# Optimization experiments

Measured on AMD Instinct MI355X. Metric: run time of the kernel, lower is better.

## Reference

```python
import jax, jax.numpy as jnp
import numpy as np

F, N, C, H, M = 256, 400, 128, 8, 128  # frames, batch*joints, mdl_channels, heads, max_pos
E = C // H


def _layer_norm(z, g, b, eps=1e-5):
    mu = jnp.mean(z, axis=-1, keepdims=True)
    var = jnp.mean((z - mu) ** 2, axis=-1, keepdims=True)
    return (z - mu) * jax.lax.rsqrt(var + eps) * g + b


def setup_inputs() -> dict:
    key = jax.random.key(0)
    ks = jax.random.split(key, 16)
    s = 0.02
    return {
        "x": jax.random.normal(ks[0], (F, N, C), jnp.float32),
        "tree_encoding": jax.random.normal(ks[1], (N, C), jnp.float32),
        "W_qkv": jax.random.normal(ks[2], (3 * C, C), jnp.float32) * s,      # Linear weight (out,in), no bias
        "W_tree_k": jax.random.normal(ks[3], (C, C), jnp.float32) * s,
        "W_tree_v": jax.random.normal(ks[4], (C, C), jnp.float32) * s,
        "emb": jax.random.normal(ks[5], (2 * M + 1, E), jnp.float32) * s,    # distance embedding table
        "W_beta": jax.random.normal(ks[6], (1, 3 * C), jnp.float32) * s,     # lin_beta (out,in), no bias
        "ln1_g": jnp.ones((C,), jnp.float32),
        "ln1_b": jnp.zeros((C,), jnp.float32),
        "ln2_g": jnp.ones((C,), jnp.float32),
        "ln2_b": jnp.zeros((C,), jnp.float32),
        "W1": jax.random.normal(ks[7], (C, C), jnp.float32) * s,
        "b1": jnp.zeros((C,), jnp.float32),
        "W2": jax.random.normal(ks[8], (C, C), jnp.float32) * s,
        "b2": jnp.zeros((C,), jnp.float32),
    }


def reference(x, tree_encoding, W_qkv, W_tree_k, W_tree_v, emb, W_beta,
              ln1_g, ln1_b, ln2_g, ln2_b, W1, b1, W2, b2):
    f, n, c = x.shape
    # qkv projection, no bias
    qkv = x @ W_qkv.T                          # (f, n, 3c)
    q, k, v = jnp.split(qkv, 3, axis=-1)       # each (f, n, c)
    # tree positional encoding added to key/value
    k = k + (tree_encoding @ W_tree_k)[None]
    v = v + (tree_encoding @ W_tree_v)[None]
    # (f, n, c) -> (n, f, h, e): n is the attention batch, f is sequence length
    to_heads = lambda t: t.transpose(1, 0, 2).reshape(n, f, H, E)
    qh, kh, vh = to_heads(q), to_heads(k), to_heads(v)
    # content scores
    qk = jnp.einsum('nlhe,nshe->nhls', qh, kh)
    # relative position bias
    ids = jnp.arange(f)
    dist = jnp.clip(ids[:, None] - ids[None, :], -M, M) + M   # (f, f)
    pe = emb[dist]                                            # (f, f, e)
    qk = qk + jnp.einsum('nlhe,lse->nhls', qh, pe)
    qk = qk + jnp.einsum('nshe,lse->nhls', kh, pe)
    scale = 1.0 / (E ** 0.5)
    att = jax.nn.softmax(qk * scale, axis=-1)                 # (n, h, f, f)
    out = jnp.einsum('nhls,nshe->nlhe', att, vh)              # (n, f, h, e)
    y = out.reshape(n, f, c).transpose(1, 0, 2)               # (f, n, c)
    # gated AddNorm (beta=True): x is residual, y is attention output
    gate = jax.nn.sigmoid(jnp.concatenate([y, x, y - x], axis=-1) @ W_beta.T)
    h1 = _layer_norm(gate * x + (1.0 - gate) * y, ln1_g, ln1_b)
    # FFN (GELU exact, as torch nn.GELU default)
    ff = jax.nn.gelu(h1 @ W1.T + b1, approximate=False) @ W2.T + b2
    return _layer_norm(ff + h1, ln2_g, ln2_b)
```

## Files before the change

### kernel.cpp

```cpp
#include <hip/hip_runtime.h>
#include <math.h>

#define F_DIM 256
#define N_DIM 400
#define C_DIM 128
#define H_DIM 8
#define E_DIM 16
#define ROWS  (F_DIM * N_DIM)
#define SBUF  (N_DIM * H_DIM * F_DIM * E_DIM)

#define S_SCALE 0.6005612043932249f

typedef _Float16 half2_t __attribute__((ext_vector_type(2)));
typedef _Float16 f16x8   __attribute__((ext_vector_type(8)));
typedef float    f32x16  __attribute__((ext_vector_type(16)));
typedef float    f32x4   __attribute__((ext_vector_type(4)));

struct H2x4 { half2_t h[4]; };

__device__ inline f16x8 pack8(float4 a, float4 b) {
    H2x4 t;
    t.h[0] = __builtin_bit_cast(half2_t, __builtin_amdgcn_cvt_pkrtz(a.x, a.y));
    t.h[1] = __builtin_bit_cast(half2_t, __builtin_amdgcn_cvt_pkrtz(a.z, a.w));
    t.h[2] = __builtin_bit_cast(half2_t, __builtin_amdgcn_cvt_pkrtz(b.x, b.y));
    t.h[3] = __builtin_bit_cast(half2_t, __builtin_amdgcn_cvt_pkrtz(b.z, b.w));
    return __builtin_bit_cast(f16x8, t);
}

__device__ inline _Float16 h_rtz(float v) {
    half2_t p = __builtin_bit_cast(half2_t, __builtin_amdgcn_cvt_pkrtz(v, v));
    return p[0];
}

__device__ inline int iclamp256(int v) { return v < 0 ? 0 : (v > 256 ? 256 : v); }

__global__ __launch_bounds__(256) void prep_pack(
    const float* __restrict__ x, const float* __restrict__ Wq,
    const float* __restrict__ emb, const float* __restrict__ te,
    const float* __restrict__ Wtk, const float* __restrict__ Wtv,
    const float* __restrict__ W1, const float* __restrict__ W2,
    _Float16* __restrict__ xh, _Float16* __restrict__ Wqh,
    _Float16* __restrict__ embh, float* __restrict__ tk, float* __restrict__ tv,
    _Float16* __restrict__ W1h, _Float16* __restrict__ W2h)
{
    int bid = blockIdx.x;
    int t   = threadIdx.x;
    if (bid < 6400) {
        int i = (bid * 256 + t) * 8;
        const float4* s = (const float4*)(x + i);
        *(uint4*)(xh + i) = __builtin_bit_cast(uint4, pack8(s[0], s[1]));
    } else if (bid < 6424) {
        int i = ((bid - 6400) * 256 + t) * 8;
        const float4* s = (const float4*)(Wq + i);
        *(uint4*)(Wqh + i) = __builtin_bit_cast(uint4, pack8(s[0], s[1]));
    } else if (bid < 6426) {
        int r = (bid - 6424) * 256 + t;
        if (r > 256) return;
        const float4* er = (const float4*)(emb + r * 16);
        float4 e0 = er[0], e1 = er[1], e2 = er[2], e3 = er[3];
        e0.x *= S_SCALE; e0.y *= S_SCALE; e0.z *= S_SCALE; e0.w *= S_SCALE;
        e1.x *= S_SCALE; e1.y *= S_SCALE; e1.z *= S_SCALE; e1.w *= S_SCALE;
        e2.x *= S_SCALE; e2.y *= S_SCALE; e2.z *= S_SCALE; e2.w *= S_SCALE;
        e3.x *= S_SCALE; e3.y *= S_SCALE; e3.z *= S_SCALE; e3.w *= S_SCALE;
        *(uint4*)(embh + r * 16)     = __builtin_bit_cast(uint4, pack8(e0, e1));
        *(uint4*)(embh + r * 16 + 8) = __builtin_bit_cast(uint4, pack8(e2, e3));
    } else if (bid < 6826) {
        int n = bid - 6426;
        const float* W = (t < 128) ? Wtk : Wtv;
        float* outp    = (t < 128) ? tk : tv;
        int j = t & 127;
        float acc = 0.f;
        #pragma unroll 4
        for (int c = 0; c < 128; ++c)
            acc += te[n * 128 + c] * W[c * 128 + j];
        outp[n * 128 + j] = acc;
    } else if (bid < 6834) {
        int i = ((bid - 6826) * 256 + t) * 8;
        const float4* s = (const float4*)(W1 + i);
        *(uint4*)(W1h + i) = __builtin_bit_cast(uint4, pack8(s[0], s[1]));
    } else {
        int i = ((bid - 6834) * 256 + t) * 8;
        const float4* s = (const float4*)(W2 + i);
        *(uint4*)(W2h + i) = __builtin_bit_cast(uint4, pack8(s[0], s[1]));
    }
}

__global__ __launch_bounds__(256) void qkv_gemm(
    const _Float16* __restrict__ xh, const _Float16* __restrict__ Wqh,
    const float* __restrict__ tk, const float* __restrict__ tv,
    _Float16* __restrict__ qn, _Float16* __restrict__ kn, _Float16* __restrict__ vn)
{
    int tid  = threadIdx.x;
    int wave = tid >> 6, lane = tid & 63;
    int m32  = lane & 31, khalf = lane >> 5;

    int bid = blockIdx.x;
    int xcd = bid & 7;
    int tt  = bid >> 3;
    int cb  = tt % 6;
    int rp  = (tt / 6) * 8 + xcd;
    int row0 = rp * 64 + (wave & 1) * 32;
    int col0 = cb * 64 + (wave >> 1) * 32;

    const _Float16* xp = xh  + (row0 + m32) * 128 + khalf * 8;
    const _Float16* wp = Wqh + (col0 + m32) * 128 + khalf * 8;

    f32x16 acc;
    #pragma unroll
    for (int i = 0; i < 16; ++i) acc[i] = 0.f;

    #pragma unroll
    for (int k0 = 0; k0 < 128; k0 += 16) {
        f16x8 xa = __builtin_bit_cast(f16x8, *(const uint4*)(xp + k0));
        f16x8 wa = __builtin_bit_cast(f16x8, *(const uint4*)(wp + k0));
        acc = __builtin_amdgcn_mfma_f32_32x32x16_f16(xa, wa, acc, 0, 0, 0);
    }

    int o   = col0 + m32;
    int sec = o >> 7;
    int rem = o & 127;
    #pragma unroll
    for (int reg = 0; reg < 16; ++reg) {
        int r = row0 + (reg & 3) + 8 * (reg >> 2) + 4 * khalf;
        float val = acc[reg];
        if (sec == 0) {
            qn[r * 128 + rem] = h_rtz(val * S_SCALE);
        } else {
            int f = r / 400;
            int n = r - f * 400;
            if (sec == 1) {
                kn[r * 128 + rem] = h_rtz((val + tk[n * 128 + rem]) * S_SCALE);
            } else {
                vn[r * 128 + rem] = (_Float16)(val + tv[n * 128 + rem]);
            }
        }
    }
}

__global__ __launch_bounds__(256) void v_pack(
    const _Float16* __restrict__ vn, _Float16* __restrict__ vT)
{
    __shared__ _Float16 sm[16 * 264];
    int bn = blockIdx.x;
    int n  = bn >> 3, h = bn & 7;
    int t  = threadIdx.x;

    const uint4* src = (const uint4*)(vn + (t * 400 + n) * 128 + h * 16);
    uint4 a = src[0], b = src[1];
    union { uint4 u; _Float16 hv[8]; } ua, ub;
    ua.u = a; ub.u = b;
    #pragma unroll
    for (int e = 0; e < 8; ++e) sm[e * 264 + t]       = ua.hv[e];
    #pragma unroll
    for (int e = 0; e < 8; ++e) sm[(e + 8) * 264 + t] = ub.hv[e];
    __syncthreads();

    #pragma unroll
    for (int k = 0; k < 2; ++k) {
        int idx = (k * 256 + t) * 8;
        int e = idx >> 8, f0 = idx & 255;
        uint4 o = *(const uint4*)(sm + e * 264 + f0);
        *(uint4*)(vT + bn * 4096 + idx) = o;
    }
}

#define R2_STRIDE 258
#define PS_STRIDE 40

__global__ __launch_bounds__(512, 4) void attn_kernel(
    const _Float16* __restrict__ qb, const _Float16* __restrict__ kb,
    const _Float16* __restrict__ vb, const _Float16* __restrict__ embh,
    _Float16* __restrict__ y)
{
    __shared__ __align__(16) _Float16 R2sh[32 * R2_STRIDE];
    __shared__ __align__(16) _Float16 Psh[8 * 32 * PS_STRIDE];

    int tid  = threadIdx.x;
    int wave = tid >> 6, lane = tid & 63;
    int bid  = blockIdx.x;
    int bn   = (bid & 7) * 400 + (bid >> 3);
    int n    = bn >> 3, h = bn & 7;
    int base = bn * 4096;

    int nn  = lane & 31;
    int kh  = lane >> 5;
    int khb = (lane & 32) << 2;
    int cbase = 31 + 4 * kh - nn;
    int dbase = 4 * kh - nn;
    int q16 = (lane >> 4) & 3;

    int nat_off = n * 128 + h * 16 + kh * 8;

    f16x8 aq = __builtin_bit_cast(f16x8,
        *(const uint4*)(qb + (32 * wave + nn) * 51200 + nat_off));

    f16x8 bones;
    #pragma unroll
    for (int i = 0; i < 8; ++i) bones[i] = (_Float16)1.0f;

    f32x4 O[2];
    f32x4 Od[2];
    #pragma unroll
    for (int a = 0; a < 2; ++a)
        #pragma unroll
        for (int r = 0; r < 4; ++r) { O[a][r] = 0.f; Od[a][r] = 0.f; }

    _Float16* psw = Psh + wave * 32 * PS_STRIDE;

    for (int st = 0; st < 8; ++st) {
        f16x8 bk = __builtin_bit_cast(f16x8,
            *(const uint4*)(kb + (32 * st + nn) * 51200 + nat_off));

        auto r2tile = [&](int ct) {
            int erow = 32 * ct + nn; if (erow > 256) erow = 256;
            f16x8 be = __builtin_bit_cast(f16x8,
                *(const uint4*)(embh + erow * 16 + kh * 8));
            f32x16 c2;
            #pragma unroll
            for (int i = 0; i < 16; ++i) c2[i] = 0.f;
            c2 = __builtin_amdgcn_mfma_f32_32x32x16_f16(bk, be, c2, 0, 0, 0);
            int col = 32 * ct + nn;
            if (col <= 256) {
                #pragma unroll
                for (int r = 0; r < 16; ++r) {
                    int srow = (r & 3) + 8 * (r >> 2) + 4 * kh;
                    R2sh[srow * R2_STRIDE + col] = (_Float16)c2[r];
                }
            }
        };
        r2tile(wave);
        if (wave == (st & 7)) r2tile(8);
        __syncthreads();

        f16x8 bv = __builtin_bit_cast(f16x8,
            *(const uint4*)(vb + base + (lane & 15) * 256 + 32 * st + q16 * 8));

        int U0 = 32 * wave - 32 * st + 128;

        int br0 = iclamp256(U0 - 31 + nn);
        int br1 = iclamp256(U0 + 1 + nn);
        f16x8 be0 = __builtin_bit_cast(f16x8,
            *(const uint4*)(embh + br0 * 16 + kh * 8));
        f16x8 be1 = __builtin_bit_cast(f16x8,
            *(const uint4*)(embh + br1 * 16 + kh * 8));
        f32x16 W0, W1;
        #pragma unroll
        for (int i = 0; i < 16; ++i) { W0[i] = 0.f; W1[i] = 0.f; }
        W0 = __builtin_amdgcn_mfma_f32_32x32x16_f16(aq, be0, W0, 0, 0, 0);
        W1 = __builtin_amdgcn_mfma_f32_32x32x16_f16(aq, be1, W1, 0, 0, 0);

        half2_t b1p[8];
        #pragma unroll
        for (int r = 0; r < 16; ++r) {
            int rmr = (r & 3) + 8 * (r >> 2);
            int c   = rmr + cbase;
            int addr = ((c & 31) << 2) + khb;
            int w01 = __builtin_bit_cast(int,
                __builtin_amdgcn_cvt_pkrtz(W0[r], W1[r]));
            half2_t hh = __builtin_bit_cast(half2_t,
                __builtin_amdgcn_ds_bpermute(addr, w01));
            b1p[r >> 1][r & 1] = (c < 32) ? hh[0] : hh[1];
        }

        f32x16 S;
        #pragma unroll
        for (int i = 0; i < 16; ++i) S[i] = 0.f;
        S = __builtin_amdgcn_mfma_f32_32x32x16_f16(aq, bk, S, 0, 0, 0);

        #pragma unroll
        for (int r = 0; r < 16; ++r) {
            int rmr = (r & 3) + 8 * (r >> 2);
            float b1 = (float)b1p[r >> 1][r & 1];
            int d = iclamp256(U0 + rmr + dbase);
            float b2 = (float)R2sh[nn * R2_STRIDE + d];
            float p = __builtin_amdgcn_exp2f(S[r] + b1 + b2);
            int mloc = rmr + 4 * kh;
            psw[mloc * PS_STRIDE + nn] = (_Float16)p;
        }

        #pragma unroll
        for (int a = 0; a < 2; ++a) {
            f16x8 ap = __builtin_bit_cast(f16x8,
                *(const uint4*)(psw + (16 * a + (lane & 15)) * PS_STRIDE + q16 * 8));
            O[a]  = __builtin_amdgcn_mfma_f32_16x16x32_f16(ap, bv,    O[a],  0, 0, 0);
            Od[a] = __builtin_amdgcn_mfma_f32_16x16x32_f16(ap, bones, Od[a], 0, 0, 0);
        }
        __syncthreads();
    }

    #pragma unroll
    for (int a = 0; a < 2; ++a) {
        #pragma unroll
        for (int r = 0; r < 4; ++r) {
            int row  = q16 * 4 + r;
            int lloc = 16 * a + row;
            int lg = 32 * wave + lloc;
            y[(lg * 400 + n) * 128 + h * 16 + (lane & 15)] =
                (_Float16)(O[a][r] / Od[a][r]);
        }
    }
}

__global__ __launch_bounds__(256) void ffn_fused(
    const float* __restrict__ x, const _Float16* __restrict__ yh,
    const float* __restrict__ Wb,
    const float* __restrict__ ln1g, const float* __restrict__ ln1b,
    const _Float16* __restrict__ W1h, const float* __restrict__ b1,
    const _Float16* __restrict__ W2h, const float* __restrict__ b2,
    const float* __restrict__ ln2g, const float* __restrict__ ln2b,
    float* __restrict__ outp)
{
    __shared__ __align__(16) _Float16 h1sh[32 * 136];
    __shared__ __align__(16) _Float16 gsh[32 * 136];
    __shared__ float Cs[32 * 132];

    int tid  = threadIdx.x;
    int rloc = tid >> 3;
    int seg  = (tid & 7) * 16;
    int r    = blockIdx.x * 32 + rloc;

    float xv[16], yv[16];
    {
        const float4* xp = (const float4*)(x + r * 128 + seg);
        float4 x0 = xp[0], x1 = xp[1], x2 = xp[2], x3 = xp[3];
        xv[0]=x0.x; xv[1]=x0.y; xv[2]=x0.z; xv[3]=x0.w;
        xv[4]=x1.x; xv[5]=x1.y; xv[6]=x1.z; xv[7]=x1.w;
        xv[8]=x2.x; xv[9]=x2.y; xv[10]=x2.z; xv[11]=x2.w;
        xv[12]=x3.x; xv[13]=x3.y; xv[14]=x3.z; xv[15]=x3.w;
        const uint4* yp = (const uint4*)(yh + r * 128 + seg);
        uint4 y0 = yp[0], y1 = yp[1];
        union { uint4 u; _Float16 hv[8]; } uy0, uy1;
        uy0.u = y0; uy1.u = y1;
        #pragma unroll
        for (int j = 0; j < 8; ++j) { yv[j] = (float)uy0.hv[j]; yv[8+j] = (float)uy1.hv[j]; }
    }
    float sv = 0.f;
    {
        const float4* w0p = (const float4*)(Wb + seg);
        const float4* w1p = (const float4*)(Wb + 128 + seg);
        const float4* w2p = (const float4*)(Wb + 256 + seg);
        #pragma unroll
        for (int j4 = 0; j4 < 4; ++j4) {
            float4 w0 = w0p[j4], w1 = w1p[j4], w2 = w2p[j4];
            float* w0f = (float*)&w0; float* w1f = (float*)&w1; float* w2f = (float*)&w2;
            #pragma unroll
            for (int jj = 0; jj < 4; ++jj) {
                int j = j4 * 4 + jj;
                sv += yv[j] * w0f[jj] + xv[j] * w1f[jj] + (yv[j] - xv[j]) * w2f[jj];
            }
        }
    }
    #pragma unroll
    for (int off = 4; off > 0; off >>= 1) sv += __shfl_xor(sv, off);
    float gate = 1.0f / (1.0f + __expf(-sv));

    float z[16], s1 = 0.f, s2 = 0.f;
    #pragma unroll
    for (int j = 0; j < 16; ++j) {
        z[j] = gate * xv[j] + (1.0f - gate) * yv[j];
        s1 += z[j]; s2 += z[j] * z[j];
    }
    #pragma unroll
    for (int off = 4; off > 0; off >>= 1) {
        s1 += __shfl_xor(s1, off);
        s2 += __shfl_xor(s2, off);
    }
    float mu  = s1 * (1.0f / 128.0f);
    float var = s2 * (1.0f / 128.0f) - mu * mu;
    float rs  = rsqrtf(var + 1e-5f);

    float h1r[16];
    {
        const float4* gp = (const float4*)(ln1g + seg);
        const float4* bp = (const float4*)(ln1b + seg);
        #pragma unroll
        for (int j4 = 0; j4 < 4; ++j4) {
            float4 gv = gp[j4], bv = bp[j4];
            float* gf = (float*)&gv; float* bf = (float*)&bv;
            #pragma unroll
            for (int jj = 0; jj < 4; ++jj) {
                int j = j4 * 4 + jj;
                h1r[j] = (z[j] - mu) * rs * gf[jj] + bf[jj];
            }
        }
        #pragma unroll
        for (int j = 0; j < 8; ++j) {
            *(uint*)(h1sh + rloc * 136 + seg + 2 * j) = __builtin_bit_cast(uint,
                __builtin_amdgcn_cvt_pkrtz(h1r[2 * j], h1r[2 * j + 1]));
        }
    }
    __syncthreads();

    int wave = tid >> 6, lane = tid & 63;
    int m32  = lane & 31, khalf = lane >> 5;
    int col0 = wave * 32;
    {
        f32x16 acc;
        #pragma unroll
        for (int i = 0; i < 16; ++i) acc[i] = 0.f;
        const _Float16* ap = h1sh + m32 * 136 + khalf * 8;
        const _Float16* wp = W1h + (col0 + m32) * 128 + khalf * 8;
        #pragma unroll
        for (int k0 = 0; k0 < 128; k0 += 16) {
            f16x8 aa = __builtin_bit_cast(f16x8, *(const uint4*)(ap + k0));
            f16x8 wa = __builtin_bit_cast(f16x8, *(const uint4*)(wp + k0));
            acc = __builtin_amdgcn_mfma_f32_32x32x16_f16(aa, wa, acc, 0, 0, 0);
        }
        int   c  = col0 + m32;
        float bi = b1[c];
        #pragma unroll
        for (int reg = 0; reg < 16; ++reg) {
            int row2 = (reg & 3) + 8 * (reg >> 2) + 4 * khalf;
            float v = acc[reg] + bi;
            v = 0.5f * v * (1.0f + erff(v * 0.70710678118654752f));
            gsh[row2 * 136 + c] = (_Float16)v;
        }
    }
    __syncthreads();

    {
        f32x16 acc;
        #pragma unroll
        for (int i = 0; i < 16; ++i) acc[i] = 0.f;
        const _Float16* ap = gsh + m32 * 136 + khalf * 8;
        const _Float16* wp = W2h + (col0 + m32) * 128 + khalf * 8;
        #pragma unroll
        for (int k0 = 0; k0 < 128; k0 += 16) {
            f16x8 aa = __builtin_bit_cast(f16x8, *(const uint4*)(ap + k0));
            f16x8 wa = __builtin_bit_cast(f16x8, *(const uint4*)(wp + k0));
            acc = __builtin_amdgcn_mfma_f32_32x32x16_f16(aa, wa, acc, 0, 0, 0);
        }
        #pragma unroll
        for (int reg = 0; reg < 16; ++reg) {
            int row2 = (reg & 3) + 8 * (reg >> 2) + 4 * khalf;
            Cs[row2 * 132 + col0 + m32] = acc[reg];
        }
    }
    __syncthreads();

    float z2[16];
    float t1 = 0.f, t2 = 0.f;
    #pragma unroll
    for (int j4 = 0; j4 < 4; ++j4) {
        float4 cv = *(const float4*)(Cs + rloc * 132 + seg + j4 * 4);
        float4 bv = *(const float4*)(b2 + seg + j4 * 4);
        float* cf = (float*)&cv; float* bf = (float*)&bv;
        #pragma unroll
        for (int jj = 0; jj < 4; ++jj) {
            int j = j4 * 4 + jj;
            z2[j] = cf[jj] + bf[jj] + h1r[j];
            t1 += z2[j]; t2 += z2[j] * z2[j];
        }
    }
    #pragma unroll
    for (int off = 4; off > 0; off >>= 1) {
        t1 += __shfl_xor(t1, off);
        t2 += __shfl_xor(t2, off);
    }
    float mu2  = t1 * (1.0f / 128.0f);
    float var2 = t2 * (1.0f / 128.0f) - mu2 * mu2;
    float rs2  = rsqrtf(var2 + 1e-5f);
    #pragma unroll
    for (int j4 = 0; j4 < 4; ++j4) {
        float4 gv = *(const float4*)(ln2g + seg + j4 * 4);
        float4 bv = *(const float4*)(ln2b + seg + j4 * 4);
        float* gf = (float*)&gv; float* bf = (float*)&bv;
        float4 ov;
        float* of = (float*)&ov;
        #pragma unroll
        for (int jj = 0; jj < 4; ++jj) {
            int j = j4 * 4 + jj;
            of[jj] = (z2[j] - mu2) * rs2 * gf[jj] + bf[jj];
        }
        *(float4*)(outp + r * 128 + seg + j4 * 4) = ov;
    }
}

extern "C" void kernel_launch(void* const* d_in, const int* in_sizes, int n_in,
                              void* d_out, int out_size, void* d_ws, size_t ws_size,
                              hipStream_t stream)
{
    const float* x     = (const float*)d_in[0];
    const float* te    = (const float*)d_in[1];
    const float* Wqkv  = (const float*)d_in[2];
    const float* Wtk   = (const float*)d_in[3];
    const float* Wtv   = (const float*)d_in[4];
    const float* emb   = (const float*)d_in[5];
    const float* Wbeta = (const float*)d_in[6];
    const float* ln1g  = (const float*)d_in[7];
    const float* ln1b  = (const float*)d_in[8];
    const float* ln2g  = (const float*)d_in[9];
    const float* ln2b  = (const float*)d_in[10];
    const float* W1    = (const float*)d_in[11];
    const float* b1    = (const float*)d_in[12];
    const float* W2    = (const float*)d_in[13];
    const float* b2    = (const float*)d_in[14];
    float* outp = (float*)d_out;

    float* ws = (float*)d_ws;
    float* tk = ws;
    float* tv = ws + 51200;
    float* qb_region = ws + 102400;
    float* kb_region = qb_region + SBUF;
    float* vb_region = kb_region + SBUF;
    float* yb        = vb_region + SBUF;

    _Float16* qnat = (_Float16*)qb_region;
    _Float16* knat = (_Float16*)kb_region;
    _Float16* vnat = (_Float16*)vb_region;
    _Float16* vT   = (_Float16*)(vb_region + SBUF / 2);
    _Float16* embh = (_Float16*)(qb_region + SBUF / 2);
    _Float16* yh   = (_Float16*)yb;
    _Float16* xh   = (_Float16*)(kb_region + SBUF / 2);
    _Float16* Wqh  = (_Float16*)(yb + SBUF / 2);
    _Float16* W1h  = (_Float16*)(yb + SBUF / 2 + 32768);
    _Float16* W2h  = (_Float16*)(yb + SBUF / 2 + 49152);

    prep_pack<<<6842, 256, 0, stream>>>(x, Wqkv, emb, te, Wtk, Wtv, W1, W2,
                                        xh, Wqh, embh, tk, tv, W1h, W2h);
    qkv_gemm<<<9600, 256, 0, stream>>>(xh, Wqh, tk, tv, qnat, knat, vnat);
    v_pack<<<3200, 256, 0, stream>>>(vnat, vT);
    attn_kernel<<<3200, 512, 0, stream>>>(qnat, knat, vT, embh, yh);
    ffn_fused<<<3200, 256, 0, stream>>>(x, yh, Wbeta, ln1g, ln1b,
                                        W1h, b1, W2h, b2, ln2g, ln2b, outp);
}
```

Baseline: 458.5 us.

## Fuse V transpose into attention kernel and double-buffer R2 to drop a barrier

Removes the separate v_pack kernel. Each attention block now loads its own V slice from the natural layout and transposes it into shared memory, so the global round trip of the transposed V buffer and one launch go away. The relative-position R2 shared buffer is double-buffered by iteration parity, which allows removing the trailing __syncthreads in the frame loop. In exchange, shared memory per block grows by roughly 25 KB, which may cut resident blocks per CU below the launch-bounds target.

```diff
diff --git a/kernel.cpp b/kernel.cpp
--- a/kernel.cpp
+++ b/kernel.cpp
@@ -137,50 +137,24 @@
     }
 }
 
-__global__ __launch_bounds__(256) void v_pack(
-    const _Float16* __restrict__ vn, _Float16* __restrict__ vT)
-{
-    __shared__ _Float16 sm[16 * 264];
-    int bn = blockIdx.x;
-    int n  = bn >> 3, h = bn & 7;
-    int t  = threadIdx.x;
-
-    const uint4* src = (const uint4*)(vn + (t * 400 + n) * 128 + h * 16);
-    uint4 a = src[0], b = src[1];
-    union { uint4 u; _Float16 hv[8]; } ua, ub;
-    ua.u = a; ub.u = b;
-    #pragma unroll
-    for (int e = 0; e < 8; ++e) sm[e * 264 + t]       = ua.hv[e];
-    #pragma unroll
-    for (int e = 0; e < 8; ++e) sm[(e + 8) * 264 + t] = ub.hv[e];
-    __syncthreads();
-
-    #pragma unroll
-    for (int k = 0; k < 2; ++k) {
-        int idx = (k * 256 + t) * 8;
-        int e = idx >> 8, f0 = idx & 255;
-        uint4 o = *(const uint4*)(sm + e * 264 + f0);
-        *(uint4*)(vT + bn * 4096 + idx) = o;
-    }
-}
-
 #define R2_STRIDE 258
 #define PS_STRIDE 40
+#define VT_STRIDE 264
 
 __global__ __launch_bounds__(512, 4) void attn_kernel(
     const _Float16* __restrict__ qb, const _Float16* __restrict__ kb,
-    const _Float16* __restrict__ vb, const _Float16* __restrict__ embh,
+    const _Float16* __restrict__ vn, const _Float16* __restrict__ embh,
     _Float16* __restrict__ y)
 {
-    __shared__ __align__(16) _Float16 R2sh[32 * R2_STRIDE];
+    __shared__ __align__(16) _Float16 R2sh[2][32 * R2_STRIDE];
     __shared__ __align__(16) _Float16 Psh[8 * 32 * PS_STRIDE];
+    __shared__ __align__(16) _Float16 VshT[16 * VT_STRIDE];
 
     int tid  = threadIdx.x;
     int wave = tid >> 6, lane = tid & 63;
     int bid  = blockIdx.x;
     int bn   = (bid & 7) * 400 + (bid >> 3);
     int n    = bn >> 3, h = bn & 7;
-    int base = bn * 4096;
 
     int nn  = lane & 31;
     int kh  = lane >> 5;
@@ -191,6 +165,15 @@
 
     int nat_off = n * 128 + h * 16 + kh * 8;
 
+    {
+        int f = tid >> 1, part = tid & 1;
+        uint4 vv = *(const uint4*)(vn + (f * 400 + n) * 128 + h * 16 + part * 8);
+        union { uint4 u; _Float16 hv[8]; } uv; uv.u = vv;
+        #pragma unroll
+        for (int j = 0; j < 8; ++j)
+            VshT[(part * 8 + j) * VT_STRIDE + f] = uv.hv[j];
+    }
+
     f16x8 aq = __builtin_bit_cast(f16x8,
         *(const uint4*)(qb + (32 * wave + nn) * 51200 + nat_off));
 
@@ -208,6 +191,8 @@
     _Float16* psw = Psh + wave * 32 * PS_STRIDE;
 
     for (int st = 0; st < 8; ++st) {
+        _Float16* R2cur = &R2sh[st & 1][0];
+
         f16x8 bk = __builtin_bit_cast(f16x8,
             *(const uint4*)(kb + (32 * st + nn) * 51200 + nat_off));
 
@@ -224,7 +209,7 @@
                 #pragma unroll
                 for (int r = 0; r < 16; ++r) {
                     int srow = (r & 3) + 8 * (r >> 2) + 4 * kh;
-                    R2sh[srow * R2_STRIDE + col] = (_Float16)c2[r];
+                    R2cur[srow * R2_STRIDE + col] = (_Float16)c2[r];
                 }
             }
         };
@@ -233,7 +218,7 @@
         __syncthreads();
 
         f16x8 bv = __builtin_bit_cast(f16x8,
-            *(const uint4*)(vb + base + (lane & 15) * 256 + 32 * st + q16 * 8));
+            *(const uint4*)(VshT + (lane & 15) * VT_STRIDE + 32 * st + q16 * 8));
 
         int U0 = 32 * wave - 32 * st + 128;
 
@@ -272,7 +257,7 @@
             int rmr = (r & 3) + 8 * (r >> 2);
             float b1 = (float)b1p[r >> 1][r & 1];
             int d = iclamp256(U0 + rmr + dbase);
-            float b2 = (float)R2sh[nn * R2_STRIDE + d];
+            float b2 = (float)R2cur[nn * R2_STRIDE + d];
             float p = __builtin_amdgcn_exp2f(S[r] + b1 + b2);
             int mloc = rmr + 4 * kh;
             psw[mloc * PS_STRIDE + nn] = (_Float16)p;
@@ -285,7 +270,6 @@
             O[a]  = __builtin_amdgcn_mfma_f32_16x16x32_f16(ap, bv,    O[a],  0, 0, 0);
             Od[a] = __builtin_amdgcn_mfma_f32_16x16x32_f16(ap, bones, Od[a], 0, 0, 0);
         }
-        __syncthreads();
     }
 
     #pragma unroll
@@ -508,7 +492,6 @@
     _Float16* qnat = (_Float16*)qb_region;
     _Float16* knat = (_Float16*)kb_region;
     _Float16* vnat = (_Float16*)vb_region;
-    _Float16* vT   = (_Float16*)(vb_region + SBUF / 2);
     _Float16* embh = (_Float16*)(qb_region + SBUF / 2);
     _Float16* yh   = (_Float16*)yb;
     _Float16* xh   = (_Float16*)(kb_region + SBUF / 2);
@@ -519,8 +502,7 @@
     prep_pack<<<6842, 256, 0, stream>>>(x, Wqkv, emb, te, Wtk, Wtv, W1, W2,
                                         xh, Wqh, embh, tk, tv, W1h, W2h);
     qkv_gemm<<<9600, 256, 0, stream>>>(xh, Wqh, tk, tv, qnat, knat, vnat);
-    v_pack<<<3200, 256, 0, stream>>>(vnat, vT);
-    attn_kernel<<<3200, 512, 0, stream>>>(qnat, knat, vT, embh, yh);
+    attn_kernel<<<3200, 512, 0, stream>>>(qnat, knat, vnat, embh, yh);
     ffn_fused<<<3200, 256, 0, stream>>>(x, yh, Wbeta, ln1g, ln1b,
                                         W1h, b1, W2h, b2, ln2g, ln2b, outp);
 }
```

Result: faster. 426.2 us (-7.0%).
